# Kernel tuning notes

Measured on AMD Instinct MI355X. Metric: run time of the kernel, lower is better.

The kernel has to match this reference:

```python
import jax, jax.numpy as jnp
import numpy as np

B, L, H, P = 16, 4096, 512, 256
LN_EPS = 1e-6  # flax nnx.LayerNorm default


def setup_inputs() -> dict:
    key = jax.random.key(0)
    ks = jax.random.split(key, 9)
    dt_min, dt_max = 1e-3, 1e-1
    x = jax.random.normal(ks[0], (B, L, H), dtype=jnp.float32)
    # lecun-normal-like scaling for B (fan_in = H) and C (fan_in = P)
    return {
        "x": x,
        "log_lambda_re": jax.random.normal(ks[1], (P,), dtype=jnp.float32),
        "lambda_im": jax.random.normal(ks[2], (P,), dtype=jnp.float32) * 3.0,
        "B_re": jax.random.normal(ks[3], (P, H), dtype=jnp.float32) / np.sqrt(H),
        "B_im": jax.random.normal(ks[4], (P, H), dtype=jnp.float32) / np.sqrt(H),
        "C_re": jax.random.normal(ks[5], (H, P), dtype=jnp.float32) / np.sqrt(P),
        "C_im": jax.random.normal(ks[6], (H, P), dtype=jnp.float32) / np.sqrt(P),
        "D": jax.random.normal(ks[7], (H,), dtype=jnp.float32),
        "log_step": jax.random.uniform(ks[8], (P,), dtype=jnp.float32)
        * (np.log(dt_max) - np.log(dt_min)) + np.log(dt_min),
        "ln_scale": jnp.ones((H,), dtype=jnp.float32),
        "ln_bias": jnp.zeros((H,), dtype=jnp.float32),
    }


def _binary_operator(q_i, q_j):
    A_i, b_i = q_i
    A_j, b_j = q_j
    return (A_j * A_i, A_j * b_i + b_j)


def reference(x, log_lambda_re, lambda_im, B_re, B_im, C_re, C_im, D, log_step,
              ln_scale, ln_bias):
    Lambda = -jnp.exp(log_lambda_re) + 1j * lambda_im          # [P] complex
    B_tilde = B_re + 1j * B_im                                  # [P,H]
    C_tilde = C_re + 1j * C_im                                  # [H,P]
    step = jnp.exp(log_step)                                    # [P]
    # ZOH discretization
    Lambda_bar = jnp.exp(Lambda * step)                         # [P]
    B_bar = ((Lambda_bar - 1.0) / Lambda)[:, None] * B_tilde    # [P,H]
    # SSM via parallel associative scan over the length axis
    Bu = x @ B_bar.T                                            # [B,L,P] complex
    Lambda_el = jnp.broadcast_to(Lambda_bar, Bu.shape)          # [B,L,P]
    _, xs = jax.lax.associative_scan(_binary_operator, (Lambda_el, Bu), axis=-2)
    ys = 2.0 * (xs @ C_tilde.T).real                            # [B,L,H]
    y = ys + x * D
    y = jax.nn.gelu(y)
    # residual + LayerNorm
    z = x + y
    mean = jnp.mean(z, axis=-1, keepdims=True)
    var = jnp.var(z, axis=-1, keepdims=True)
    return (z - mean) * jax.lax.rsqrt(var + LN_EPS) * ln_scale + ln_bias
```

## Files before the change

kernel.cpp:

```cpp
#include <hip/hip_runtime.h>
#include <hip/hip_bf16.h>
#include <cstdint>
#include <cstddef>

typedef short bf16x8 __attribute__((ext_vector_type(8)));
typedef float f32x4  __attribute__((ext_vector_type(4)));

#define HH 512
#define PP 256
#define LL 4096
#define BBATCH 16
#define MM (BBATCH * LL)
#define NCHUNK 128
#define SCHUNK 32

__device__ __forceinline__ unsigned short f2bf(float f) {
  union { float f; unsigned u; } v; v.f = f;
  unsigned r = (v.u + 0x7FFFu + ((v.u >> 16) & 1u)) >> 16;
  return (unsigned short)r;
}
__device__ __forceinline__ float bf2f(unsigned short b) {
  return __uint_as_float(((unsigned)b) << 16);
}

__device__ __forceinline__ void async16(const void* g, void* l) {
  __builtin_amdgcn_global_load_lds(
      (const __attribute__((address_space(1))) unsigned*)g,
      (__attribute__((address_space(3))) unsigned*)l, 16, 0, 0);
}

__global__ void precompute_params(const float* __restrict__ llr_,
                                  const float* __restrict__ lim_,
                                  const float* __restrict__ lstep_,
                                  float* __restrict__ lam) {
  int p = threadIdx.x;
  if (p >= PP) return;
  float Lr = -expf(llr_[p]);
  float Li = lim_[p];
  float st = expf(lstep_[p]);
  float mag = expf(Lr * st);
  float ang = Li * st;
  float lbr = mag * cosf(ang);
  float lbi = mag * sinf(ang);
  float den = Lr * Lr + Li * Li;
  float nr = lbr - 1.f, ni = lbi;
  float cr = (nr * Lr + ni * Li) / den;
  float ci = (ni * Lr - nr * Li) / den;
  float m32 = expf(32.f * Lr * st);
  float a32r = m32 * cosf(32.f * ang);
  float a32i = m32 * sinf(32.f * ang);
  lam[p]            = lbr;
  lam[PP + p]       = lbi;
  lam[2 * PP + p]   = a32r;
  lam[3 * PP + p]   = a32i;
  lam[4 * PP + p]   = cr;
  lam[5 * PP + p]   = ci;
}

__global__ void build_weights(const float* __restrict__ B_re,
                              const float* __restrict__ B_im,
                              const float* __restrict__ C_re,
                              const float* __restrict__ C_im,
                              const float* __restrict__ lam,
                              unsigned short* __restrict__ Bcat,
                              unsigned short* __restrict__ Ccat) {
  int bid = blockIdx.x;
  int tid = threadIdx.x;
  if (bid < 512) {
    int n = bid;
    int p = (n < PP) ? n : n - PP;
    float cr = lam[4 * PP + p], ci = lam[5 * PP + p];
    for (int c = tid; c < HH; c += 256) {
      float br = B_re[(size_t)p * HH + c];
      float bi = B_im[(size_t)p * HH + c];
      float v = (n < PP) ? (cr * br - ci * bi) : (cr * bi + ci * br);
      Bcat[(size_t)n * HH + c] = f2bf(v);
    }
  } else {
    int h = bid - 512;
    for (int c = tid; c < HH; c += 256) {
      float v = (c < PP) ? 2.f * C_re[(size_t)h * PP + c]
                         : -2.f * C_im[(size_t)h * PP + (c - PP)];
      Ccat[(size_t)h * HH + c] = f2bf(v);
    }
  }
}

__global__ __launch_bounds__(256) void cvt_x_bf16(const float* __restrict__ x,
                                                  unsigned short* __restrict__ xb) {
  const float4* x4 = (const float4*)x;
  ushort4* o4 = (ushort4*)xb;
  int stride = 2048 * 256;
  for (int i = blockIdx.x * 256 + threadIdx.x; i < (MM * HH / 4); i += stride) {
    float4 v = x4[i];
    ushort4 o;
    o.x = f2bf(v.x); o.y = f2bf(v.y); o.z = f2bf(v.z); o.w = f2bf(v.w);
    o4[i] = o;
  }
}

template <int EPI>
__global__ __launch_bounds__(256) void gemm_bt(const unsigned short* __restrict__ A,
                                               const unsigned short* __restrict__ Bt,
                                               const float* __restrict__ xf,
                                               const float* __restrict__ Dv,
                                               unsigned short* __restrict__ Cout) {
  __shared__ __align__(16) unsigned short Asl[128 * 64];
  __shared__ __align__(16) unsigned short Bsl[128 * 64];
  const int tid = threadIdx.x, lane = tid & 63, w = tid >> 6;
  const int bid = blockIdx.x;
  const int mt = bid >> 2, nt = bid & 3;
  const int m0 = mt * 128, n0 = nt * 128;
  const int r = lane & 15, g = lane >> 4;
  const int wm = (w >> 1) * 64, wn = (w & 1) * 64;

  f32x4 acc[4][4];
#pragma unroll
  for (int a = 0; a < 4; ++a)
#pragma unroll
    for (int b = 0; b < 4; ++b) acc[a][b] = (f32x4){0.f, 0.f, 0.f, 0.f};

  for (int kt = 0; kt < 512; kt += 64) {
#pragma unroll
    for (int j = 0; j < 4; ++j) {
      int idx = w * 4 + j;
      int linear = (idx * 64 + lane) * 8;
      int row = linear >> 6;
      int col = linear & 63;
      async16(A + (size_t)(m0 + row) * 512 + kt + col, &Asl[idx * 512 + lane * 8]);
      async16(Bt + (size_t)(n0 + row) * 512 + kt + col, &Bsl[idx * 512 + lane * 8]);
    }
    asm volatile("s_waitcnt vmcnt(0)" ::: "memory");
    __syncthreads();
#pragma unroll
    for (int kk = 0; kk < 2; ++kk) {
      bf16x8 af[4], bv[4];
#pragma unroll
      for (int mi = 0; mi < 4; ++mi)
        af[mi] = *(const bf16x8*)&Asl[(wm + mi * 16 + r) * 64 + kk * 32 + g * 8];
#pragma unroll
      for (int ni = 0; ni < 4; ++ni)
        bv[ni] = *(const bf16x8*)&Bsl[(wn + ni * 16 + r) * 64 + kk * 32 + g * 8];
#pragma unroll
      for (int mi = 0; mi < 4; ++mi)
#pragma unroll
        for (int ni = 0; ni < 4; ++ni)
          acc[mi][ni] = __builtin_amdgcn_mfma_f32_16x16x32_bf16(
              af[mi], bv[ni], acc[mi][ni], 0, 0, 0);
    }
    __syncthreads();
  }

#pragma unroll
  for (int mi = 0; mi < 4; ++mi) {
#pragma unroll
    for (int ni = 0; ni < 4; ++ni) {
      int col = n0 + wn + ni * 16 + r;
      float Dh = (EPI == 1) ? Dv[col] : 0.f;
#pragma unroll
      for (int j = 0; j < 4; ++j) {
        int row = m0 + wm + mi * 16 + g * 4 + j;
        float v = acc[mi][ni][j];
        if (EPI == 0) {
          Cout[(size_t)row * 512 + col] = f2bf(v);
        } else {
          float xv = xf[(size_t)row * 512 + col];
          float t = v + xv * Dh;
          float u = 0.7978845608028654f * (t + 0.044715f * t * t * t);
          float e = __expf(2.f * u);
          float th = 1.f - 2.f / (e + 1.f);
          float y = 0.5f * t * (1.f + th);
          Cout[(size_t)row * 512 + col] = f2bf(xv + y);
        }
      }
    }
  }
}

__global__ __launch_bounds__(256) void scan_carry(const unsigned short* __restrict__ Bu,
                                                  const float* __restrict__ lam,
                                                  float* __restrict__ carry) {
  int bid = blockIdx.x;
  int b = bid >> 7, c = bid & 127;
  int p = threadIdx.x;
  float ar = lam[p], ai = lam[PP + p];
  float sr = 0.f, si = 0.f;
  size_t base = ((size_t)b * LL + (size_t)c * SCHUNK) * 512;
#pragma unroll
  for (int i = 0; i < SCHUNK; ++i) {
    float ur = bf2f(Bu[base + (size_t)i * 512 + p]);
    float ui = bf2f(Bu[base + (size_t)i * 512 + 256 + p]);
    float nr = ar * sr - ai * si + ur;
    float ni = ar * si + ai * sr + ui;
    sr = nr; si = ni;
  }
  carry[(size_t)bid * 512 + p] = sr;
  carry[(size_t)bid * 512 + 256 + p] = si;
}

__global__ void scan_chain(float* __restrict__ carry, const float* __restrict__ lam) {
  int b = blockIdx.x;
  int p = threadIdx.x;
  float a32r = lam[2 * PP + p], a32i = lam[3 * PP + p];
  float sr = 0.f, si = 0.f;
  for (int c = 0; c < NCHUNK; ++c) {
    size_t idx = (size_t)(b * NCHUNK + c) * 512;
    float cr = carry[idx + p], ci = carry[idx + 256 + p];
    carry[idx + p] = sr;
    carry[idx + 256 + p] = si;
    float nr = cr + a32r * sr - a32i * si;
    float ni = ci + a32r * si + a32i * sr;
    sr = nr; si = ni;
  }
}

__global__ __launch_bounds__(256) void scan_final(const unsigned short* __restrict__ Bu,
                                                  const float* __restrict__ lam,
                                                  const float* __restrict__ carry,
                                                  unsigned short* __restrict__ xs) {
  int bid = blockIdx.x;
  int b = bid >> 7, c = bid & 127;
  int p = threadIdx.x;
  float ar = lam[p], ai = lam[PP + p];
  size_t cidx = (size_t)bid * 512;
  float sr = carry[cidx + p], si = carry[cidx + 256 + p];
  size_t base = ((size_t)b * LL + (size_t)c * SCHUNK) * 512;
#pragma unroll
  for (int i = 0; i < SCHUNK; ++i) {
    float ur = bf2f(Bu[base + (size_t)i * 512 + p]);
    float ui = bf2f(Bu[base + (size_t)i * 512 + 256 + p]);
    float nr = ar * sr - ai * si + ur;
    float ni = ar * si + ai * sr + ui;
    sr = nr; si = ni;
    xs[base + (size_t)i * 512 + p] = f2bf(sr);
    xs[base + (size_t)i * 512 + 256 + p] = f2bf(si);
  }
}

__global__ __launch_bounds__(256) void ln_kernel(const unsigned short* __restrict__ z,
                                                 const float* __restrict__ scale,
                                                 const float* __restrict__ bias,
                                                 float* __restrict__ out) {
  int tid = threadIdx.x, lane = tid & 63, wv = tid >> 6;
  int gw = blockIdx.x * 4 + wv;
  int c0 = lane * 8;
  float sc[8], bi[8];
#pragma unroll
  for (int j = 0; j < 8; ++j) { sc[j] = scale[c0 + j]; bi[j] = bias[c0 + j]; }
  for (int row = gw; row < MM; row += 8192) {
    uint4 zv = *(const uint4*)(z + (size_t)row * 512 + c0);
    float f[8];
    f[0] = __uint_as_float(zv.x << 16); f[1] = __uint_as_float(zv.x & 0xFFFF0000u);
    f[2] = __uint_as_float(zv.y << 16); f[3] = __uint_as_float(zv.y & 0xFFFF0000u);
    f[4] = __uint_as_float(zv.z << 16); f[5] = __uint_as_float(zv.z & 0xFFFF0000u);
    f[6] = __uint_as_float(zv.w << 16); f[7] = __uint_as_float(zv.w & 0xFFFF0000u);
    float s = 0.f, s2 = 0.f;
#pragma unroll
    for (int j = 0; j < 8; ++j) { s += f[j]; s2 += f[j] * f[j]; }
#pragma unroll
    for (int o = 32; o; o >>= 1) {
      s += __shfl_xor(s, o, 64);
      s2 += __shfl_xor(s2, o, 64);
    }
    float mean = s * (1.f / 512.f);
    float var = s2 * (1.f / 512.f) - mean * mean;
    float inv = rsqrtf(var + 1e-6f);
    float o8[8];
#pragma unroll
    for (int j = 0; j < 8; ++j) o8[j] = (f[j] - mean) * inv * sc[j] + bi[j];
    float4* op = (float4*)(out + (size_t)row * 512 + c0);
    op[0] = make_float4(o8[0], o8[1], o8[2], o8[3]);
    op[1] = make_float4(o8[4], o8[5], o8[6], o8[7]);
  }
}

extern "C" void kernel_launch(void* const* d_in, const int* in_sizes, int n_in,
                              void* d_out, int out_size, void* d_ws, size_t ws_size,
                              hipStream_t stream) {
  const float* x    = (const float*)d_in[0];
  const float* llr  = (const float*)d_in[1];
  const float* lim  = (const float*)d_in[2];
  const float* B_re = (const float*)d_in[3];
  const float* B_im = (const float*)d_in[4];
  const float* C_re = (const float*)d_in[5];
  const float* C_im = (const float*)d_in[6];
  const float* Dv   = (const float*)d_in[7];
  const float* lstep= (const float*)d_in[8];
  const float* lnsc = (const float*)d_in[9];
  const float* lnbi = (const float*)d_in[10];
  float* out = (float*)d_out;

  char* ws = (char*)d_ws;
  unsigned short* xb   = (unsigned short*)(ws);
  unsigned short* bu   = (unsigned short*)(ws + 67108864);
  unsigned short* bcat = (unsigned short*)(ws + 134217728);
  unsigned short* ccat = (unsigned short*)(ws + 134742016);
  float* lam           = (float*)(ws + 135266304);
  float* carry         = (float*)(ws + 135272448);

  precompute_params<<<1, 256, 0, stream>>>(llr, lim, lstep, lam);
  build_weights<<<1024, 256, 0, stream>>>(B_re, B_im, C_re, C_im, lam, bcat, ccat);
  cvt_x_bf16<<<2048, 256, 0, stream>>>(x, xb);
  gemm_bt<0><<<2048, 256, 0, stream>>>(xb, bcat, nullptr, nullptr, bu);
  scan_carry<<<2048, 256, 0, stream>>>(bu, lam, carry);
  scan_chain<<<16, 256, 0, stream>>>(carry, lam);
  scan_final<<<2048, 256, 0, stream>>>(bu, lam, carry, xb);
  gemm_bt<1><<<2048, 256, 0, stream>>>(xb, ccat, x, Dv, bu);
  ln_kernel<<<2048, 256, 0, stream>>>(bu, lnsc, lnbi, out);
}
```

Measured before the change: 475.1 us.

## Swizzle GEMM LDS tiles, remap blocks, reuse bf16 x and buffers in place

Applies an XOR swizzle to the 128-byte LDS rows in the bf16 GEMM so the MFMA fragment reads avoid bank conflicts. It also remaps block IDs so that consecutive blocks are spread across the 8 XCDs. The second GEMM epilogue now reads x from the bf16 copy instead of fp32, which halves that traffic but lowers the precision of the residual and D term. The scan writes its result in place over Bu, and the GEMM writes its output over the bf16 x buffer, so __restrict__ is dropped on the aliased pointers. That aliasing is safe only because each element is read before it is written.

After: 476.5 us. Within noise of the previous version (+0.3%).

```diff
diff --git a/kernel.cpp b/kernel.cpp
--- a/kernel.cpp
+++ b/kernel.cpp
@@ -102,33 +102,41 @@
 template <int EPI>
 __global__ __launch_bounds__(256) void gemm_bt(const unsigned short* __restrict__ A,
                                                const unsigned short* __restrict__ Bt,
-                                               const float* __restrict__ xf,
+                                               const unsigned short* xf,
                                                const float* __restrict__ Dv,
-                                               unsigned short* __restrict__ Cout) {
+                                               unsigned short* Cout) {
   __shared__ __align__(16) unsigned short Asl[128 * 64];
   __shared__ __align__(16) unsigned short Bsl[128 * 64];
   const int tid = threadIdx.x, lane = tid & 63, w = tid >> 6;
   const int bid = blockIdx.x;
-  const int mt = bid >> 2, nt = bid & 3;
+  const int logical = (bid & 7) * 256 + (bid >> 3);
+  const int mt = logical >> 2, nt = logical & 3;
   const int m0 = mt * 128, n0 = nt * 128;
   const int r = lane & 15, g = lane >> 4;
   const int wm = (w >> 1) * 64, wn = (w & 1) * 64;
 
+  const char* Ab = (const char*)A;
+  const char* Bb = (const char*)Bt;
+  char* AslB = (char*)Asl;
+  char* BslB = (char*)Bsl;
+
   f32x4 acc[4][4];
 #pragma unroll
   for (int a = 0; a < 4; ++a)
 #pragma unroll
     for (int b = 0; b < 4; ++b) acc[a][b] = (f32x4){0.f, 0.f, 0.f, 0.f};
+
+  const int swz = (r & 7) << 4;
 
   for (int kt = 0; kt < 512; kt += 64) {
 #pragma unroll
     for (int j = 0; j < 4; ++j) {
       int idx = w * 4 + j;
-      int linear = (idx * 64 + lane) * 8;
-      int row = linear >> 6;
-      int col = linear & 63;
-      async16(A + (size_t)(m0 + row) * 512 + kt + col, &Asl[idx * 512 + lane * 8]);
-      async16(Bt + (size_t)(n0 + row) * 512 + kt + col, &Bsl[idx * 512 + lane * 8]);
+      int W = idx * 1024 + lane * 16;
+      int row = W >> 7;
+      int colb = (W & 127) ^ ((row & 7) << 4);
+      async16(Ab + (size_t)(m0 + row) * 1024 + kt * 2 + colb, AslB + W);
+      async16(Bb + (size_t)(n0 + row) * 1024 + kt * 2 + colb, BslB + W);
     }
     asm volatile("s_waitcnt vmcnt(0)" ::: "memory");
     __syncthreads();
@@ -137,10 +145,12 @@
       bf16x8 af[4], bv[4];
 #pragma unroll
       for (int mi = 0; mi < 4; ++mi)
-        af[mi] = *(const bf16x8*)&Asl[(wm + mi * 16 + r) * 64 + kk * 32 + g * 8];
+        af[mi] = *(const bf16x8*)(AslB + (wm + mi * 16 + r) * 128 +
+                                  ((kk * 64 + g * 16) ^ swz));
 #pragma unroll
       for (int ni = 0; ni < 4; ++ni)
-        bv[ni] = *(const bf16x8*)&Bsl[(wn + ni * 16 + r) * 64 + kk * 32 + g * 8];
+        bv[ni] = *(const bf16x8*)(BslB + (wn + ni * 16 + r) * 128 +
+                                  ((kk * 64 + g * 16) ^ swz));
 #pragma unroll
       for (int mi = 0; mi < 4; ++mi)
 #pragma unroll
@@ -164,7 +174,7 @@
         if (EPI == 0) {
           Cout[(size_t)row * 512 + col] = f2bf(v);
         } else {
-          float xv = xf[(size_t)row * 512 + col];
+          float xv = bf2f(xf[(size_t)row * 512 + col]);
           float t = v + xv * Dh;
           float u = 0.7978845608028654f * (t + 0.044715f * t * t * t);
           float e = __expf(2.f * u);
@@ -214,10 +224,10 @@
   }
 }
 
-__global__ __launch_bounds__(256) void scan_final(const unsigned short* __restrict__ Bu,
+__global__ __launch_bounds__(256) void scan_final(const unsigned short* Bu,
                                                   const float* __restrict__ lam,
                                                   const float* __restrict__ carry,
-                                                  unsigned short* __restrict__ xs) {
+                                                  unsigned short* xs) {
   int bid = blockIdx.x;
   int b = bid >> 7, c = bid & 127;
   int p = threadIdx.x;
@@ -304,7 +314,7 @@
   gemm_bt<0><<<2048, 256, 0, stream>>>(xb, bcat, nullptr, nullptr, bu);
   scan_carry<<<2048, 256, 0, stream>>>(bu, lam, carry);
   scan_chain<<<16, 256, 0, stream>>>(carry, lam);
-  scan_final<<<2048, 256, 0, stream>>>(bu, lam, carry, xb);
-  gemm_bt<1><<<2048, 256, 0, stream>>>(xb, ccat, x, Dv, bu);
-  ln_kernel<<<2048, 256, 0, stream>>>(bu, lnsc, lnbi, out);
-}
+  scan_final<<<2048, 256, 0, stream>>>(bu, lam, carry, bu);
+  gemm_bt<1><<<2048, 256, 0, stream>>>(bu, ccat, xb, Dv, xb);
+  ln_kernel<<<2048, 256, 0, stream>>>(xb, lnsc, lnbi, out);
+}
```
